# Kernel tuning notes

Measured on AMD Instinct MI355X. Metric: run time of the kernel, lower is better.

## Reference

```python
import jax, jax.numpy as jnp
import numpy as np

N_NODES = 100000


def gcn_conv(x, src, dst, W, b):
    # PyG GCNConv: linear transform first, then symmetric-normalized aggregation.
    h = x @ W  # [N, out]
    ones = jnp.ones(dst.shape[0], dtype=x.dtype)
    deg = jax.ops.segment_sum(ones, dst, num_segments=N_NODES)  # in-degree incl. self-loops
    dinv = jnp.where(deg > 0, jax.lax.rsqrt(deg), 0.0)
    norm = dinv[src] * dinv[dst]  # [E]
    msg = h[src] * norm[:, None]  # gather + scale
    out = jax.ops.segment_sum(msg, dst, num_segments=N_NODES)  # scatter-add
    return out + b


def add_self_loops(edge_index):
    loops = jnp.arange(N_NODES, dtype=edge_index.dtype)
    src = jnp.concatenate([edge_index[0], loops])
    dst = jnp.concatenate([edge_index[1], loops])
    return src, dst


def setup_inputs() -> dict:
    key = jax.random.key(0)
    k1, k2, k3, k4 = jax.random.split(key, 4)
    N, F, H, C, E = N_NODES, 512, 16, 40, 3200000
    x = jax.random.normal(k1, (N, F), dtype=jnp.float32)
    edge_index = jax.random.randint(k2, (2, E), 0, N, dtype=jnp.int64)
    W1 = jax.random.normal(k3, (F, H), dtype=jnp.float32) * (1.0 / np.sqrt(F))
    b1 = jnp.zeros((H,), dtype=jnp.float32)
    W2 = jax.random.normal(k4, (H, C), dtype=jnp.float32) * (1.0 / np.sqrt(H))
    b2 = jnp.zeros((C,), dtype=jnp.float32)
    return {"x": x, "edge_index": edge_index, "W1": W1, "b1": b1, "W2": W2, "b2": b2}


def reference(x, edge_index, W1, b1, W2, b2):
    src, dst = add_self_loops(edge_index)
    h = gcn_conv(x, src, dst, W1, b1)
    h = jax.nn.relu(h)
    logits = gcn_conv(h, src, dst, W2, b2)
    return jax.nn.log_softmax(logits, axis=1), logits
```

## Files before the change

### kernel.cpp

```cpp
#include <hip/hip_runtime.h>
#include <hip/hip_bf16.h>
#include <math.h>

#define N_NODES 100000
#define F_IN 512
#define H_DIM 16
#define C_DIM 40

#define BSHIFT 9
#define BNODES 512
#define NBUCK 196
#define CHUNK 8192
#define SRC_MASK 0x1FFFF

#define KSPLIT 4
#define KSEG (F_IN / KSPLIT)


__global__ void __launch_bounds__(256) bhist_kernel(const int* __restrict__ dst,
                                                    int* __restrict__ BC, int E) {
    __shared__ int cnt[NBUCK];
    int start = blockIdx.x * CHUNK;
    int end = start + CHUNK < E ? start + CHUNK : E;
    for (int i = threadIdx.x; i < NBUCK; i += 256) cnt[i] = 0;
    __syncthreads();
    for (int i = start + threadIdx.x; i < end; i += 256)
        atomicAdd(&cnt[dst[i] >> BSHIFT], 1);
    __syncthreads();
    for (int i = threadIdx.x; i < NBUCK; i += 256) {
        int c = cnt[i];
        if (c) atomicAdd(&BC[i], c);
    }
}


__global__ void __launch_bounds__(256) bscan_kernel(const int* __restrict__ BC,
                                                    int* __restrict__ BO,
                                                    int* __restrict__ cursor,
                                                    int* __restrict__ R, int E, int N) {
    __shared__ int buf[2][256];
    int tid = threadIdx.x;
    int v = (tid < NBUCK) ? BC[tid] : 0;
    int cur = 0;
    buf[0][tid] = v;
    __syncthreads();
    for (int off = 1; off < 256; off <<= 1) {
        int t = buf[cur][tid] + ((tid >= off) ? buf[cur][tid - off] : 0);
        cur ^= 1;
        buf[cur][tid] = t;
        __syncthreads();
    }
    int excl = buf[cur][tid] - v;
    if (tid <= NBUCK) {
        BO[tid] = excl;
        if (tid < NBUCK) cursor[tid] = excl;
    }
    if (tid == 0) R[N] = E;
}


__global__ void __launch_bounds__(256) partition_kernel(const int* __restrict__ src,
                                                        const int* __restrict__ dst,
                                                        int* __restrict__ cursor,
                                                        int* __restrict__ packed, int E) {
    __shared__ int cnt[NBUCK];
    __shared__ int base[NBUCK];
    int start = blockIdx.x * CHUNK;
    int end = start + CHUNK < E ? start + CHUNK : E;
    for (int i = threadIdx.x; i < NBUCK; i += 256) cnt[i] = 0;
    __syncthreads();
    for (int i = start + threadIdx.x; i < end; i += 256)
        atomicAdd(&cnt[dst[i] >> BSHIFT], 1);
    __syncthreads();
    for (int i = threadIdx.x; i < NBUCK; i += 256) {
        int c = cnt[i];
        base[i] = c ? atomicAdd(&cursor[i], c) : 0;
        cnt[i] = 0;
    }
    __syncthreads();
    for (int i = start + threadIdx.x; i < end; i += 256) {
        int d = dst[i];
        int b = d >> BSHIFT;
        int p = base[b] + atomicAdd(&cnt[b], 1);
        packed[p] = ((d & (BNODES - 1)) << 17) | src[i];
    }
}


__global__ void __launch_bounds__(512) sort2_kernel(const int* __restrict__ BO,
                                                    const int* __restrict__ packed,
                                                    int* __restrict__ R,
                                                    float* __restrict__ dinv,
                                                    int* __restrict__ eidx, int N) {
    __shared__ int cnt[BNODES];
    __shared__ int buf[2][BNODES];
    int b = blockIdx.x;
    int tid = threadIdx.x;
    int lo = BO[b], hi = BO[b + 1];
    cnt[tid] = 0;
    __syncthreads();
    for (int e = lo + tid; e < hi; e += 512)
        atomicAdd(&cnt[packed[e] >> 17], 1);
    __syncthreads();
    int deg = cnt[tid];
    int cur = 0;
    buf[0][tid] = deg;
    __syncthreads();
    for (int off = 1; off < 512; off <<= 1) {
        int t = buf[cur][tid] + ((tid >= off) ? buf[cur][tid - off] : 0);
        cur ^= 1;
        buf[cur][tid] = t;
        __syncthreads();
    }
    int excl = lo + buf[cur][tid] - deg;
    int n = (b << BSHIFT) + tid;
    if (n < N) {
        R[n] = excl;
        dinv[n] = rsqrtf((float)(deg + 1));
    }
    cnt[tid] = excl;
    __syncthreads();
    for (int e = lo + tid; e < hi; e += 512) {
        int p = packed[e];
        int pos = atomicAdd(&cnt[p >> 17], 1);
        eidx[pos] = p & SRC_MASK;
    }
}


#define G1_ISSUE(BUF, KC)                                            \
    {                                                                \
        _Pragma("unroll")                                            \
        for (int p = 0; p < 4; ++p) BUF[p] = xr[(KC) * 4 + p];       \
    }

#define G1_COMPUTE(BUF, KC)                                          \
    {                                                                \
        const float4* Wk = (const float4*)(Wb + (KC) * 16 * H_DIM);  \
        const float* xf = (const float*)BUF;                         \
        _Pragma("unroll")                                            \
        for (int j = 0; j < 16; ++j) {                               \
            float s = xf[j];                                         \
            _Pragma("unroll")                                        \
            for (int p = 0; p < 4; ++p) {                            \
                float4 wv = Wk[j * 4 + p];                           \
                acc[4 * p + 0] += s * wv.x;                          \
                acc[4 * p + 1] += s * wv.y;                          \
                acc[4 * p + 2] += s * wv.z;                          \
                acc[4 * p + 3] += s * wv.w;                          \
            }                                                        \
        }                                                            \
    }

__global__ void __launch_bounds__(64) gemm1p_kernel(const float* __restrict__ x,
                                                    const float* __restrict__ W1,
                                                    float* __restrict__ part, int N) {
    int bid = blockIdx.x;
    int ks = bid & (KSPLIT - 1);
    int rb = bid >> 2;
    int row = rb * 64 + threadIdx.x;
    int cr = row < N ? row : N - 1;
    const float4* xr = (const float4*)(x + (size_t)cr * F_IN + ks * KSEG);
    const float* Wb = W1 + ks * KSEG * H_DIM;

    float4 bufA[4], bufB[4];
    float acc[H_DIM];
#pragma unroll
    for (int k = 0; k < H_DIM; k++) acc[k] = 0.0f;

    G1_ISSUE(bufA, 0);
#pragma unroll
    for (int kc = 0; kc < KSEG / 16; kc += 2) {
        G1_ISSUE(bufB, kc + 1);
        G1_COMPUTE(bufA, kc);
        if (kc + 2 < KSEG / 16) G1_ISSUE(bufA, kc + 2);
        G1_COMPUTE(bufB, kc + 1);
    }

    if (row < N) {
        float4* o = (float4*)(part + (size_t)ks * N * H_DIM + (size_t)row * H_DIM);
#pragma unroll
        for (int p = 0; p < 4; p++)
            o[p] = make_float4(acc[4 * p], acc[4 * p + 1], acc[4 * p + 2], acc[4 * p + 3]);
    }
}


__global__ void __launch_bounds__(256) g1red_kernel(const float* __restrict__ part,
                                                    const float* __restrict__ dinv,
                                                    float* __restrict__ g1, int N) {
    int t = blockIdx.x * 256 + threadIdx.x;
    int total = N * H_DIM / 4;
    if (t >= total) return;
    const float4* p = (const float4*)part;
    float4 a = p[t];
    float4 b = p[t + (size_t)total];
    float4 c = p[t + (size_t)2 * total];
    float4 d = p[t + (size_t)3 * total];
    float di = dinv[t >> 2];
    ((float4*)g1)[t] = make_float4(di * (((a.x + b.x) + c.x) + d.x),
                                   di * (((a.y + b.y) + c.y) + d.y),
                                   di * (((a.z + b.z) + c.z) + d.z),
                                   di * (((a.w + b.w) + c.w) + d.w));
}


__global__ void __launch_bounds__(256) agg1_kernel(const int* __restrict__ R,
                                                   const int* __restrict__ eidx,
                                                   const float* __restrict__ g1,
                                                   const float* __restrict__ dinv,
                                                   const float* __restrict__ b1,
                                                   float* __restrict__ g2, int N) {
    int t = blockIdx.x * 256 + threadIdx.x;
    int n = t >> 4;
    if (n >= N) return;
    int k = t & 15;
    int lo = R[n], hi = R[n + 1];
    float sum = g1[t];
    int e = lo;
    for (; e + 8 <= hi; e += 8) {
        int s[8];
        float v[8];
#pragma unroll
        for (int u = 0; u < 8; u++) s[u] = eidx[e + u];
#pragma unroll
        for (int u = 0; u < 8; u++) v[u] = g1[s[u] * H_DIM + k];
#pragma unroll
        for (int u = 0; u < 8; u++) sum += v[u];
    }
    for (; e < hi; ++e) sum += g1[eidx[e] * H_DIM + k];
    float di = dinv[n];
    g2[t] = di * fmaxf(di * sum + b1[k], 0.0f);
}

__global__ void __launch_bounds__(256) agg2_kernel(const int* __restrict__ R,
                                                   const int* __restrict__ eidx,
                                                   const float* __restrict__ g2,
                                                   float* __restrict__ s2, int N) {
    int t = blockIdx.x * 256 + threadIdx.x;
    int n = t >> 4;
    if (n >= N) return;
    int k = t & 15;
    int lo = R[n], hi = R[n + 1];
    float sum = g2[t];
    int e = lo;
    for (; e + 8 <= hi; e += 8) {
        int s[8];
        float v[8];
#pragma unroll
        for (int u = 0; u < 8; u++) s[u] = eidx[e + u];
#pragma unroll
        for (int u = 0; u < 8; u++) v[u] = g2[s[u] * H_DIM + k];
#pragma unroll
        for (int u = 0; u < 8; u++) sum += v[u];
    }
    for (; e < hi; ++e) sum += g2[eidx[e] * H_DIM + k];
    s2[t] = sum;
}


__global__ void __launch_bounds__(256) final_kernel(const float* __restrict__ s2,
                                                    const float* __restrict__ dinv,
                                                    const float* __restrict__ W2,
                                                    const float* __restrict__ b2,
                                                    float* __restrict__ out, int N) {
    __shared__ float w2s[H_DIM * C_DIM];
    __shared__ float b2s[C_DIM];
    __shared__ float stage[256 * 41];
    for (int i = threadIdx.x; i < H_DIM * C_DIM; i += 256) w2s[i] = W2[i];
    if (threadIdx.x < C_DIM) b2s[threadIdx.x] = b2[threadIdx.x];
    __syncthreads();
    int n = blockIdx.x * 256 + threadIdx.x;
    int cn = n < N ? n : 0;
    float di = dinv[cn];
    float v[H_DIM];
    const float4* sv = (const float4*)(s2 + (size_t)cn * H_DIM);
#pragma unroll
    for (int p = 0; p < 4; p++) {
        float4 t = sv[p];
        v[4 * p] = di * t.x; v[4 * p + 1] = di * t.y;
        v[4 * p + 2] = di * t.z; v[4 * p + 3] = di * t.w;
    }
    float lg[C_DIM];
    float m = -1e30f;
    for (int c = 0; c < C_DIM; c++) {
        float a = b2s[c];
#pragma unroll
        for (int k = 0; k < H_DIM; k++) a += v[k] * w2s[k * C_DIM + c];
        lg[c] = a;
        m = fmaxf(m, a);
    }
    float ssum = 0.0f;
    for (int c = 0; c < C_DIM; c++) ssum += __expf(lg[c] - m);
    float lse = m + __logf(ssum);

    size_t base = (size_t)blockIdx.x * 256 * C_DIM;
    size_t lim = (size_t)N * C_DIM;
    for (int c = 0; c < C_DIM; c++) stage[threadIdx.x * 41 + c] = lg[c] - lse;
    __syncthreads();
    for (int i = threadIdx.x; i < 256 * C_DIM; i += 256) {
        int nn = i / C_DIM, c = i - nn * C_DIM;
        size_t g = base + i;
        if (g < lim) out[g] = stage[nn * 41 + c];
    }
    __syncthreads();
    for (int c = 0; c < C_DIM; c++) stage[threadIdx.x * 41 + c] = lg[c];
    __syncthreads();
    for (int i = threadIdx.x; i < 256 * C_DIM; i += 256) {
        int nn = i / C_DIM, c = i - nn * C_DIM;
        size_t g = base + i;
        if (g < lim) out[lim + g] = stage[nn * 41 + c];
    }
}


extern "C" void kernel_launch(void* const* d_in, const int* in_sizes, int n_in,
                              void* d_out, int out_size, void* d_ws, size_t ws_size,
                              hipStream_t stream) {
    const float* x  = (const float*)d_in[0];
    const int* ei   = (const int*)d_in[1];
    const float* W1 = (const float*)d_in[2];
    const float* b1 = (const float*)d_in[3];
    const float* W2 = (const float*)d_in[4];
    const float* b2 = (const float*)d_in[5];
    float* out = (float*)d_out;

    const int N = N_NODES;
    const int E = in_sizes[1] / 2;
    const int* src = ei;
    const int* dst = ei + E;

    int* R      = (int*)d_ws;
    int* BC     = R + 100016;
    int* BO     = BC + 512;
    int* cursor = BO + 256;
    float* dinv = (float*)(cursor + 256);
    int* eidx   = (int*)(dinv + 100016);
    int* packed = eidx + E;
    float* g1   = (float*)packed;
    float* g2   = g1 + 16 * N;
    float* s2   = g1;
    float* part = g2 + 16 * N;

    const int NB = (N + 255) / 256;
    const int NCH = (E + CHUNK - 1) / CHUNK;
    const int NRB = (N + 63) / 64;

    hipMemsetAsync(BC, 0, NBUCK * sizeof(int), stream);
    bhist_kernel<<<NCH, 256, 0, stream>>>(dst, BC, E);
    bscan_kernel<<<1, 256, 0, stream>>>(BC, BO, cursor, R, E, N);
    partition_kernel<<<NCH, 256, 0, stream>>>(src, dst, cursor, packed, E);
    sort2_kernel<<<NBUCK, 512, 0, stream>>>(BO, packed, R, dinv, eidx, N);

    gemm1p_kernel<<<NRB * KSPLIT, 64, 0, stream>>>(x, W1, part, N);
    g1red_kernel<<<(N * H_DIM / 4 + 255) / 256, 256, 0, stream>>>(part, dinv, g1, N);
    agg1_kernel<<<(N * 16 + 255) / 256, 256, 0, stream>>>(R, eidx, g1, dinv, b1, g2, N);
    agg2_kernel<<<(N * 16 + 255) / 256, 256, 0, stream>>>(R, eidx, g2, s2, N);
    final_kernel<<<NB, 256, 0, stream>>>(s2, dinv, W2, b2, out, N);
}
```

Baseline: 531.4 us.

## Fuse layer-2 aggregation with final GEMM/log-softmax; retune sort2 and gemm1 blocks

Merges the agg2 and final kernels into one fin2 kernel. Each group of 16 threads aggregates one node's features into shared memory, then computes the 40 logits and log-softmax with wave shuffles, which drops the s2 round trip and one launch. sort2 now runs with 1024 threads per block, and gemm1p uses 256-thread blocks with larger 8-float4 load batches and a fully unrolled two-buffer schedule. Risks include more register pressure in gemm1p and uncoalesced 16-wide output stores in fin2. fin2 also assumes N is divisible by 16, because it drops the n<N bounds check.

Result: no change. 530.7 us (-0.1%).

```diff
diff --git a/kernel.cpp b/kernel.cpp
--- a/kernel.cpp
+++ b/kernel.cpp
@@ -87,40 +87,43 @@
 }
 
 
-__global__ void __launch_bounds__(512) sort2_kernel(const int* __restrict__ BO,
-                                                    const int* __restrict__ packed,
-                                                    int* __restrict__ R,
-                                                    float* __restrict__ dinv,
-                                                    int* __restrict__ eidx, int N) {
+__global__ void __launch_bounds__(1024) sort2_kernel(const int* __restrict__ BO,
+                                                     const int* __restrict__ packed,
+                                                     int* __restrict__ R,
+                                                     float* __restrict__ dinv,
+                                                     int* __restrict__ eidx, int N) {
     __shared__ int cnt[BNODES];
     __shared__ int buf[2][BNODES];
     int b = blockIdx.x;
     int tid = threadIdx.x;
     int lo = BO[b], hi = BO[b + 1];
-    cnt[tid] = 0;
-    __syncthreads();
-    for (int e = lo + tid; e < hi; e += 512)
+    if (tid < BNODES) cnt[tid] = 0;
+    __syncthreads();
+    for (int e = lo + tid; e < hi; e += 1024)
         atomicAdd(&cnt[packed[e] >> 17], 1);
     __syncthreads();
-    int deg = cnt[tid];
+    int deg = (tid < BNODES) ? cnt[tid] : 0;
     int cur = 0;
-    buf[0][tid] = deg;
-    __syncthreads();
-    for (int off = 1; off < 512; off <<= 1) {
-        int t = buf[cur][tid] + ((tid >= off) ? buf[cur][tid - off] : 0);
+    if (tid < BNODES) buf[0][tid] = deg;
+    __syncthreads();
+    for (int off = 1; off < BNODES; off <<= 1) {
+        int t = 0;
+        if (tid < BNODES) t = buf[cur][tid] + ((tid >= off) ? buf[cur][tid - off] : 0);
         cur ^= 1;
-        buf[cur][tid] = t;
+        if (tid < BNODES) buf[cur][tid] = t;
         __syncthreads();
     }
-    int excl = lo + buf[cur][tid] - deg;
-    int n = (b << BSHIFT) + tid;
-    if (n < N) {
-        R[n] = excl;
-        dinv[n] = rsqrtf((float)(deg + 1));
-    }
-    cnt[tid] = excl;
-    __syncthreads();
-    for (int e = lo + tid; e < hi; e += 512) {
+    if (tid < BNODES) {
+        int excl = lo + buf[cur][tid] - deg;
+        int n = (b << BSHIFT) + tid;
+        if (n < N) {
+            R[n] = excl;
+            dinv[n] = rsqrtf((float)(deg + 1));
+        }
+        cnt[tid] = excl;
+    }
+    __syncthreads();
+    for (int e = lo + tid; e < hi; e += 1024) {
         int p = packed[e];
         int pos = atomicAdd(&cnt[p >> 17], 1);
         eidx[pos] = p & SRC_MASK;
@@ -128,22 +131,22 @@
 }
 
 
-#define G1_ISSUE(BUF, KC)                                            \
+#define G1_ISSUE(BUF, G)                                             \
     {                                                                \
         _Pragma("unroll")                                            \
-        for (int p = 0; p < 4; ++p) BUF[p] = xr[(KC) * 4 + p];       \
-    }
-
-#define G1_COMPUTE(BUF, KC)                                          \
+        for (int p = 0; p < 8; ++p) BUF[p] = xr[(G) * 8 + p];        \
+    }
+
+#define G1_COMPUTE(BUF, G)                                           \
     {                                                                \
-        const float4* Wk = (const float4*)(Wb + (KC) * 16 * H_DIM);  \
-        const float* xf = (const float*)BUF;                         \
+        const float* xf = (const float*)(BUF);                       \
         _Pragma("unroll")                                            \
-        for (int j = 0; j < 16; ++j) {                               \
+        for (int j = 0; j < 32; ++j) {                               \
             float s = xf[j];                                         \
+            const float4* Wj = (const float4*)(Wb + ((G) * 32 + j) * H_DIM); \
             _Pragma("unroll")                                        \
             for (int p = 0; p < 4; ++p) {                            \
-                float4 wv = Wk[j * 4 + p];                           \
+                float4 wv = Wj[p];                                   \
                 acc[4 * p + 0] += s * wv.x;                          \
                 acc[4 * p + 1] += s * wv.y;                          \
                 acc[4 * p + 2] += s * wv.z;                          \
@@ -152,30 +155,30 @@
         }                                                            \
     }
 
-__global__ void __launch_bounds__(64) gemm1p_kernel(const float* __restrict__ x,
-                                                    const float* __restrict__ W1,
-                                                    float* __restrict__ part, int N) {
+__global__ void __launch_bounds__(256) gemm1p_kernel(const float* __restrict__ x,
+                                                     const float* __restrict__ W1,
+                                                     float* __restrict__ part, int N) {
     int bid = blockIdx.x;
     int ks = bid & (KSPLIT - 1);
     int rb = bid >> 2;
-    int row = rb * 64 + threadIdx.x;
+    int row = rb * 256 + threadIdx.x;
     int cr = row < N ? row : N - 1;
     const float4* xr = (const float4*)(x + (size_t)cr * F_IN + ks * KSEG);
     const float* Wb = W1 + ks * KSEG * H_DIM;
 
-    float4 bufA[4], bufB[4];
+    float4 bufA[8], bufB[8];
     float acc[H_DIM];
 #pragma unroll
     for (int k = 0; k < H_DIM; k++) acc[k] = 0.0f;
 
     G1_ISSUE(bufA, 0);
-#pragma unroll
-    for (int kc = 0; kc < KSEG / 16; kc += 2) {
-        G1_ISSUE(bufB, kc + 1);
-        G1_COMPUTE(bufA, kc);
-        if (kc + 2 < KSEG / 16) G1_ISSUE(bufA, kc + 2);
-        G1_COMPUTE(bufB, kc + 1);
-    }
+    G1_ISSUE(bufB, 1);
+    G1_COMPUTE(bufA, 0);
+    G1_ISSUE(bufA, 2);
+    G1_COMPUTE(bufB, 1);
+    G1_ISSUE(bufB, 3);
+    G1_COMPUTE(bufA, 2);
+    G1_COMPUTE(bufB, 3);
 
     if (row < N) {
         float4* o = (float4*)(part + (size_t)ks * N * H_DIM + (size_t)row * H_DIM);
@@ -233,13 +236,22 @@
     g2[t] = di * fmaxf(di * sum + b1[k], 0.0f);
 }
 
-__global__ void __launch_bounds__(256) agg2_kernel(const int* __restrict__ R,
+
+__global__ void __launch_bounds__(256) fin2_kernel(const int* __restrict__ R,
                                                    const int* __restrict__ eidx,
                                                    const float* __restrict__ g2,
-                                                   float* __restrict__ s2, int N) {
+                                                   const float* __restrict__ dinv,
+                                                   const float* __restrict__ W2,
+                                                   const float* __restrict__ b2,
+                                                   float* __restrict__ out, int N) {
+    __shared__ float w2s[H_DIM * C_DIM];
+    __shared__ float b2s[C_DIM];
+    __shared__ float vsh[16][17];
+    for (int i = threadIdx.x; i < H_DIM * C_DIM; i += 256) w2s[i] = W2[i];
+    if (threadIdx.x < C_DIM) b2s[threadIdx.x] = b2[threadIdx.x];
+
     int t = blockIdx.x * 256 + threadIdx.x;
     int n = t >> 4;
-    if (n >= N) return;
     int k = t & 15;
     int lo = R[n], hi = R[n + 1];
     float sum = g2[t];
@@ -255,62 +267,42 @@
         for (int u = 0; u < 8; u++) sum += v[u];
     }
     for (; e < hi; ++e) sum += g2[eidx[e] * H_DIM + k];
-    s2[t] = sum;
-}
-
-
-__global__ void __launch_bounds__(256) final_kernel(const float* __restrict__ s2,
-                                                    const float* __restrict__ dinv,
-                                                    const float* __restrict__ W2,
-                                                    const float* __restrict__ b2,
-                                                    float* __restrict__ out, int N) {
-    __shared__ float w2s[H_DIM * C_DIM];
-    __shared__ float b2s[C_DIM];
-    __shared__ float stage[256 * 41];
-    for (int i = threadIdx.x; i < H_DIM * C_DIM; i += 256) w2s[i] = W2[i];
-    if (threadIdx.x < C_DIM) b2s[threadIdx.x] = b2[threadIdx.x];
-    __syncthreads();
-    int n = blockIdx.x * 256 + threadIdx.x;
-    int cn = n < N ? n : 0;
-    float di = dinv[cn];
-    float v[H_DIM];
-    const float4* sv = (const float4*)(s2 + (size_t)cn * H_DIM);
-#pragma unroll
-    for (int p = 0; p < 4; p++) {
-        float4 t = sv[p];
-        v[4 * p] = di * t.x; v[4 * p + 1] = di * t.y;
-        v[4 * p + 2] = di * t.z; v[4 * p + 3] = di * t.w;
-    }
-    float lg[C_DIM];
-    float m = -1e30f;
-    for (int c = 0; c < C_DIM; c++) {
-        float a = b2s[c];
-#pragma unroll
-        for (int k = 0; k < H_DIM; k++) a += v[k] * w2s[k * C_DIM + c];
-        lg[c] = a;
-        m = fmaxf(m, a);
-    }
-    float ssum = 0.0f;
-    for (int c = 0; c < C_DIM; c++) ssum += __expf(lg[c] - m);
-    float lse = m + __logf(ssum);
-
-    size_t base = (size_t)blockIdx.x * 256 * C_DIM;
+    vsh[threadIdx.x >> 4][k] = dinv[n] * sum;
+    __syncthreads();
+
+    int g = threadIdx.x >> 4;
+    int j = threadIdx.x & 15;
+    const float* v = vsh[g];
+    int c2 = (j < 8) ? 32 + j : j;
+    float lg0 = b2s[j];
+    float lg1 = b2s[j + 16];
+    float lg2 = (j < 8) ? b2s[32 + j] : -1e30f;
+    float lg2acc = 0.0f;
+#pragma unroll
+    for (int kk = 0; kk < H_DIM; ++kk) {
+        float vk = v[kk];
+        lg0 += vk * w2s[kk * C_DIM + j];
+        lg1 += vk * w2s[kk * C_DIM + j + 16];
+        lg2acc += vk * w2s[kk * C_DIM + c2];
+    }
+    if (j < 8) lg2 += lg2acc;
+
+    float m = fmaxf(fmaxf(lg0, lg1), lg2);
+#pragma unroll
+    for (int s = 1; s < 16; s <<= 1) m = fmaxf(m, __shfl_xor(m, s, 64));
+    float ss = __expf(lg0 - m) + __expf(lg1 - m) + ((j < 8) ? __expf(lg2 - m) : 0.0f);
+#pragma unroll
+    for (int s = 1; s < 16; s <<= 1) ss += __shfl_xor(ss, s, 64);
+    float lse = m + __logf(ss);
+
+    size_t base = (size_t)n * C_DIM;
     size_t lim = (size_t)N * C_DIM;
-    for (int c = 0; c < C_DIM; c++) stage[threadIdx.x * 41 + c] = lg[c] - lse;
-    __syncthreads();
-    for (int i = threadIdx.x; i < 256 * C_DIM; i += 256) {
-        int nn = i / C_DIM, c = i - nn * C_DIM;
-        size_t g = base + i;
-        if (g < lim) out[g] = stage[nn * 41 + c];
-    }
-    __syncthreads();
-    for (int c = 0; c < C_DIM; c++) stage[threadIdx.x * 41 + c] = lg[c];
-    __syncthreads();
-    for (int i = threadIdx.x; i < 256 * C_DIM; i += 256) {
-        int nn = i / C_DIM, c = i - nn * C_DIM;
-        size_t g = base + i;
-        if (g < lim) out[lim + g] = stage[nn * 41 + c];
-    }
+    out[base + j] = lg0 - lse;
+    out[base + 16 + j] = lg1 - lse;
+    if (j < 8) out[base + 32 + j] = lg2 - lse;
+    out[lim + base + j] = lg0;
+    out[lim + base + 16 + j] = lg1;
+    if (j < 8) out[lim + base + 32 + j] = lg2;
 }
 
 
@@ -339,22 +331,19 @@
     int* packed = eidx + E;
     float* g1   = (float*)packed;
     float* g2   = g1 + 16 * N;
-    float* s2   = g1;
     float* part = g2 + 16 * N;
 
     const int NB = (N + 255) / 256;
     const int NCH = (E + CHUNK - 1) / CHUNK;
-    const int NRB = (N + 63) / 64;
 
     hipMemsetAsync(BC, 0, NBUCK * sizeof(int), stream);
     bhist_kernel<<<NCH, 256, 0, stream>>>(dst, BC, E);
     bscan_kernel<<<1, 256, 0, stream>>>(BC, BO, cursor, R, E, N);
     partition_kernel<<<NCH, 256, 0, stream>>>(src, dst, cursor, packed, E);
-    sort2_kernel<<<NBUCK, 512, 0, stream>>>(BO, packed, R, dinv, eidx, N);
-
-    gemm1p_kernel<<<NRB * KSPLIT, 64, 0, stream>>>(x, W1, part, N);
+    sort2_kernel<<<NBUCK, 1024, 0, stream>>>(BO, packed, R, dinv, eidx, N);
+
+    gemm1p_kernel<<<NB * KSPLIT, 256, 0, stream>>>(x, W1, part, N);
     g1red_kernel<<<(N * H_DIM / 4 + 255) / 256, 256, 0, stream>>>(part, dinv, g1, N);
     agg1_kernel<<<(N * 16 + 255) / 256, 256, 0, stream>>>(R, eidx, g1, dinv, b1, g2, N);
-    agg2_kernel<<<(N * 16 + 255) / 256, 256, 0, stream>>>(R, eidx, g2, s2, N);
-    final_kernel<<<NB, 256, 0, stream>>>(s2, dinv, W2, b2, out, N);
-}
+    fin2_kernel<<<N / 16, 256, 0, stream>>>(R, eidx, g2, dinv, W2, b2, out, N);
+}
```
